# Kernel tuning notes

Hardware: AMD Instinct MI355X
Metric: run time of the kernel (lower is better)

## Reference

```python
import jax, jax.numpy as jnp
import numpy as np

HEAD_DIM = 128
ROPE_THETA = 10000.0


def _rope_cos_sin(positions, head_dim, theta):
    # positions: [T] int -> cos/sin [T, head_dim] (LLaMA half-split convention)
    inv_freq = 1.0 / (theta ** (jnp.arange(0, head_dim, 2, dtype=jnp.float32) / head_dim))
    ang = positions.astype(jnp.float32)[:, None] * inv_freq  # [T, D/2]
    cos = jnp.concatenate([jnp.cos(ang), jnp.cos(ang)], axis=-1)
    sin = jnp.concatenate([jnp.sin(ang), jnp.sin(ang)], axis=-1)
    return cos, sin


def _apply_rope(x, cos, sin):
    # x: [T, H, D]; rotate_half: (-x2, x1)
    half = x.shape[-1] // 2
    rot = jnp.concatenate([-x[..., half:], x[..., :half]], axis=-1)
    return x * cos[:, None, :] + rot * sin[:, None, :]


def setup_inputs() -> dict:
    key = jax.random.key(0)
    ks = jax.random.split(key, 5)
    T, hid = 4096, 4096
    S = 1024  # equal-length sequences -> B = T // S = 4
    Hq, Hk, D = 32, 8, HEAD_DIM
    hidden = jax.random.normal(ks[0], (T, hid), dtype=jnp.float32)
    positions = (jnp.arange(T, dtype=jnp.int32) % S)
    q_w = jax.random.normal(ks[1], (Hq * D, hid), dtype=jnp.float32) * 0.02
    k_w = jax.random.normal(ks[2], (Hk * D, hid), dtype=jnp.float32) * 0.02
    v_w = jax.random.normal(ks[3], (Hk * D, hid), dtype=jnp.float32) * 0.02
    o_w = jax.random.normal(ks[4], (hid, Hq * D), dtype=jnp.float32) * 0.02
    return {"hidden": hidden, "positions": positions, "q_w": q_w, "k_w": k_w,
            "v_w": v_w, "o_w": o_w, "seq_len": S}


def reference(hidden, positions, q_w, k_w, v_w, o_w, seq_len):
    T, hid = hidden.shape
    D = HEAD_DIM
    Hq = q_w.shape[0] // D
    Hk = k_w.shape[0] // D
    G = Hq // Hk  # num_kv_groups
    S = int(seq_len)
    B = T // S
    # QKV projections (ColumnParallel, tp=1): y = x @ W^T
    q = (hidden @ q_w.T).reshape(T, Hq, D)
    k = (hidden @ k_w.T).reshape(T, Hk, D)
    v = (hidden @ v_w.T).reshape(T, Hk, D)
    # fused RoPE on q and k
    cos, sin = _rope_cos_sin(positions, D, ROPE_THETA)
    q = _apply_rope(q, cos, sin)
    k = _apply_rope(k, cos, sin)
    # varlen (equal-length) causal GQA attention
    q = q.reshape(B, S, Hk, G, D)
    k = k.reshape(B, S, Hk, D)
    v = v.reshape(B, S, Hk, D)
    scale = 1.0 / np.sqrt(D).astype(np.float32)
    scores = jnp.einsum('bqhgd,bkhd->bhgqk', q, k) * scale  # [B,Hk,G,S,S]
    causal = jnp.tril(jnp.ones((S, S), dtype=bool))
    scores = jnp.where(causal, scores, jnp.asarray(-1e30, scores.dtype))
    attn = jax.nn.softmax(scores, axis=-1)
    out = jnp.einsum('bhgqk,bkhd->bqhgd', attn, v).reshape(T, Hq * D)
    # output projection (RowParallel, tp=1)
    return out @ o_w.T
```

## Files before the change

### kernel.cpp

```cpp
#include <hip/hip_runtime.h>
#include <hip/hip_bf16.h>

typedef __attribute__((ext_vector_type(8))) short bf16x8;
typedef __attribute__((ext_vector_type(4))) float f32x4;
typedef __attribute__((ext_vector_type(8))) unsigned short u16x8;

__device__ inline unsigned short f2bf(float f) {
  unsigned u = __builtin_bit_cast(unsigned, f);
  u += 0x7FFFu + ((u >> 16) & 1u);
  return (unsigned short)(u >> 16);
}
__device__ inline float b2f(unsigned short h) {
  unsigned u = ((unsigned)h) << 16;
  return __builtin_bit_cast(float, u);
}

typedef const __attribute__((address_space(1))) void* gas_ptr;
typedef __attribute__((address_space(3))) void* las_ptr;
__device__ inline void load_lds16(const void* g, void* l) {
  __builtin_amdgcn_global_load_lds((gas_ptr)g, (las_ptr)l, 16, 0, 0);
}

#define PHB() do { asm volatile("" ::: "memory"); __builtin_amdgcn_s_barrier(); \
                   __builtin_amdgcn_sched_barrier(0); } while (0)
#define PHB_MID() do { asm volatile("" ::: "memory"); __builtin_amdgcn_s_barrier(); } while (0)

__global__ __launch_bounds__(256) void cvt_f32_bf16(const float* __restrict__ src,
                                                    unsigned short* __restrict__ dst,
                                                    int n4) {
  int i = blockIdx.x * 256 + threadIdx.x;
  if (i >= n4) return;
  float4 v = ((const float4*)src)[i];
  ushort4 o;
  o.x = f2bf(v.x); o.y = f2bf(v.y); o.z = f2bf(v.z); o.w = f2bf(v.w);
  ((ushort4*)dst)[i] = o;
}

template <int NLOADS>
__device__ inline void stage_tile(const unsigned short* __restrict__ g, int ld,
                                  size_t grow0, int kcol0, char* ldsdst, int tid) {
#pragma unroll
  for (int i = 0; i < NLOADS; ++i) {
    int c = tid + i * 512;
    int r = c >> 3;
    int k = (c & 7) ^ (r & 7);
    load_lds16(g + (grow0 + r) * ld + kcol0 + k * 8, ldsdst + c * 16);
  }
}

template <int Kc, int Nc>
__global__ __launch_bounds__(512, 1) void gemmQ(const unsigned short* __restrict__ A,
                                                const unsigned short* __restrict__ B,
                                                unsigned short* __restrict__ C) {
  __shared__ __attribute__((aligned(16))) char lds[98304];
  const int tid = threadIdx.x;
  const int wave = tid >> 6, lane = tid & 63;
  const int l15 = lane & 15, l4 = lane >> 4;
  const int wr = wave >> 2, wc = wave & 3;
  const int nTN = Nc >> 8;
  const int cpx = gridDim.x >> 3;
  const int orig = blockIdx.x;
  const int wg = (orig & 7) * cpx + (orig >> 3);
  const int bm = wg / nTN, bn = wg % nTN;
  const size_t rowA0 = (size_t)bm << 7, rowB0 = (size_t)bn << 8;
  const int nt = Kc >> 6;

  stage_tile<2>(A, Kc, rowA0, 0,  lds + 0,     tid);
  stage_tile<4>(B, Kc, rowB0, 0,  lds + 16384, tid);
  stage_tile<2>(A, Kc, rowA0, 64, lds + 49152, tid);
  stage_tile<4>(B, Kc, rowB0, 64, lds + 65536, tid);
  asm volatile("s_waitcnt vmcnt(6)" ::: "memory");
  __builtin_amdgcn_s_barrier();
  __builtin_amdgcn_sched_barrier(0);

  f32x4 acc[4][4] = {};

#pragma unroll 2
  for (int t = 0; t < nt; ++t) {
    char* cbuf = lds + (t & 1) * 49152;
    const char* bufA = cbuf;
    const char* bufB = cbuf + 16384;
    const int kc2 = (t + 2) << 6;

    bf16x8 af[4][2], bf[4][2];

#pragma unroll
    for (int m = 0; m < 2; ++m) {
      int row = wr * 64 + m * 16 + l15;
#pragma unroll
      for (int kk = 0; kk < 2; ++kk)
        af[m][kk] = *(const bf16x8*)(bufA + (row << 7) + (((kk * 4 + l4) ^ (row & 7)) << 4));
    }
#pragma unroll
    for (int n = 0; n < 2; ++n) {
      int row = wc * 64 + n * 16 + l15;
#pragma unroll
      for (int kk = 0; kk < 2; ++kk)
        bf[n][kk] = *(const bf16x8*)(bufB + (row << 7) + (((kk * 4 + l4) ^ (row & 7)) << 4));
    }
    PHB_MID();
    __builtin_amdgcn_s_setprio(1);
#pragma unroll
    for (int m = 0; m < 2; ++m)
#pragma unroll
      for (int n = 0; n < 2; ++n)
#pragma unroll
        for (int kk = 0; kk < 2; ++kk)
          acc[m][n] = __builtin_amdgcn_mfma_f32_16x16x32_bf16(af[m][kk], bf[n][kk], acc[m][n], 0, 0, 0);
    __builtin_amdgcn_s_setprio(0);
    PHB();

#pragma unroll
    for (int n = 2; n < 4; ++n) {
      int row = wc * 64 + n * 16 + l15;
#pragma unroll
      for (int kk = 0; kk < 2; ++kk)
        bf[n][kk] = *(const bf16x8*)(bufB + (row << 7) + (((kk * 4 + l4) ^ (row & 7)) << 4));
    }
    PHB_MID();
    __builtin_amdgcn_s_setprio(1);
#pragma unroll
    for (int m = 0; m < 2; ++m)
#pragma unroll
      for (int n = 2; n < 4; ++n)
#pragma unroll
        for (int kk = 0; kk < 2; ++kk)
          acc[m][n] = __builtin_amdgcn_mfma_f32_16x16x32_bf16(af[m][kk], bf[n][kk], acc[m][n], 0, 0, 0);
    __builtin_amdgcn_s_setprio(0);
    PHB();

#pragma unroll
    for (int m = 2; m < 4; ++m) {
      int row = wr * 64 + m * 16 + l15;
#pragma unroll
      for (int kk = 0; kk < 2; ++kk)
        af[m][kk] = *(const bf16x8*)(bufA + (row << 7) + (((kk * 4 + l4) ^ (row & 7)) << 4));
    }
    if (t < nt - 2) stage_tile<4>(B, Kc, rowB0, kc2, cbuf + 16384, tid);
    PHB_MID();
    __builtin_amdgcn_s_setprio(1);
#pragma unroll
    for (int m = 2; m < 4; ++m)
#pragma unroll
      for (int n = 0; n < 2; ++n)
#pragma unroll
        for (int kk = 0; kk < 2; ++kk)
          acc[m][n] = __builtin_amdgcn_mfma_f32_16x16x32_bf16(af[m][kk], bf[n][kk], acc[m][n], 0, 0, 0);
    __builtin_amdgcn_s_setprio(0);
    PHB();

    if (t < nt - 2) stage_tile<2>(A, Kc, rowA0, kc2, cbuf, tid);
    if (t <= nt - 3) { asm volatile("s_waitcnt vmcnt(6)" ::: "memory"); }
    else             { asm volatile("s_waitcnt vmcnt(0)" ::: "memory"); }
    PHB_MID();
    __builtin_amdgcn_s_setprio(1);
#pragma unroll
    for (int m = 2; m < 4; ++m)
#pragma unroll
      for (int n = 2; n < 4; ++n)
#pragma unroll
        for (int kk = 0; kk < 2; ++kk)
          acc[m][n] = __builtin_amdgcn_mfma_f32_16x16x32_bf16(af[m][kk], bf[n][kk], acc[m][n], 0, 0, 0);
    __builtin_amdgcn_s_setprio(0);
    PHB();
  }

#pragma unroll
  for (int m = 0; m < 4; ++m)
#pragma unroll
    for (int n = 0; n < 4; ++n)
#pragma unroll
      for (int r = 0; r < 4; ++r) {
        size_t row = rowA0 + wr * 64 + m * 16 + l4 * 4 + r;
        size_t col = rowB0 + wc * 64 + n * 16 + l15;
        C[row * Nc + col] = f2bf(acc[m][n][r]);
      }
}

__device__ inline void stage_half(const unsigned short* __restrict__ g, int ld,
                                  size_t grow0, int kcol0, char* ldsdst, int tid) {
#pragma unroll
  for (int i = 0; i < 2; ++i) {
    int c = tid + i * 512;
    int r = c >> 3;
    int k = (c & 7) ^ (r & 7);
    load_lds16(g + (grow0 + r) * ld + kcol0 + k * 8, ldsdst + c * 16);
  }
}

template <int Kc, int Nc, bool OUT_F32>
__global__ __launch_bounds__(512, 2) void gemm8(const unsigned short* __restrict__ A,
                                                const unsigned short* __restrict__ B,
                                                void* __restrict__ Cv) {
  __shared__ __attribute__((aligned(16))) char lds[131072];
  const int tid = threadIdx.x;
  const int wave = tid >> 6, lane = tid & 63;
  const int l15 = lane & 15, l4 = lane >> 4, swz = l15 & 7;
  const int wr = wave >> 2, wc = wave & 3;
  const int nTN = Nc >> 8;
  const int cpx = gridDim.x >> 3;
  const int orig = blockIdx.x;
  const int wg = (orig & 7) * cpx + (orig >> 3);
  const int bm = wg / nTN, bn = wg % nTN;
  const size_t rowA0 = (size_t)bm << 8, rowB0 = (size_t)bn << 8;
  const int nt = Kc >> 6;
  const int brow = (wc & 1) * 64;

  stage_half(A, Kc, rowA0,       0,  lds + 0,             tid);
  stage_half(A, Kc, rowA0 + 128, 0,  lds + 16384,         tid);
  stage_half(B, Kc, rowB0,       0,  lds + 32768,         tid);
  stage_half(B, Kc, rowB0 + 128, 0,  lds + 49152,         tid);
  stage_half(B, Kc, rowB0,       64, lds + 65536 + 32768, tid);
  stage_half(A, Kc, rowA0,       64, lds + 65536,         tid);
  stage_half(A, Kc, rowA0 + 128, 64, lds + 65536 + 16384, tid);
  asm volatile("s_waitcnt vmcnt(6)" ::: "memory");
  __builtin_amdgcn_s_barrier();
  __builtin_amdgcn_sched_barrier(0);

  f32x4 acc[8][4] = {};
  bf16x8 bf01[2][2];
  {
    const char* bufB0 = lds + 32768 + (wc >> 1) * 16384;
#pragma unroll
    for (int n = 0; n < 2; ++n)
#pragma unroll
      for (int kk = 0; kk < 2; ++kk)
        bf01[n][kk] = *(const bf16x8*)(bufB0 + ((brow + n * 16 + l15) << 7) + (((kk * 4 + l4) ^ swz) << 4));
  }

#pragma unroll 2
  for (int t = 0; t < nt; ++t) {
    char* cbuf = lds + (t & 1) * 65536;
    char* obuf = lds + ((t + 1) & 1) * 65536;
    const char* bufA = cbuf + wr * 16384;
    const char* bufB = cbuf + 32768 + (wc >> 1) * 16384;
    const int kc1 = (t + 1) << 6, kc2 = (t + 2) << 6;

    bf16x8 af[8][2], bf23[2][2];

#pragma unroll
    for (int m = 0; m < 4; ++m)
#pragma unroll
      for (int kk = 0; kk < 2; ++kk)
        af[m][kk] = *(const bf16x8*)(bufA + ((m * 16 + l15) << 7) + (((kk * 4 + l4) ^ swz) << 4));
    if (t < nt - 1) stage_half(B, Kc, rowB0 + 128, kc1, obuf + 49152, tid);
    PHB_MID();
    __builtin_amdgcn_s_setprio(1);
#pragma unroll
    for (int m = 0; m < 4; ++m)
#pragma unroll
      for (int n = 0; n < 2; ++n)
#pragma unroll
        for (int kk = 0; kk < 2; ++kk)
          acc[m][n] = __builtin_amdgcn_mfma_f32_16x16x32_bf16(af[m][kk], bf01[n][kk], acc[m][n], 0, 0, 0);
    __builtin_amdgcn_s_setprio(0);
    PHB();

#pragma unroll
    for (int n = 0; n < 2; ++n)
#pragma unroll
      for (int kk = 0; kk < 2; ++kk)
        bf23[n][kk] = *(const bf16x8*)(bufB + ((brow + (n + 2) * 16 + l15) << 7) + (((kk * 4 + l4) ^ swz) << 4));
    PHB_MID();
    __builtin_amdgcn_s_setprio(1);
#pragma unroll
    for (int m = 0; m < 4; ++m)
#pragma unroll
      for (int n = 0; n < 2; ++n)
#pragma unroll
        for (int kk = 0; kk < 2; ++kk)
          acc[m][n + 2] = __builtin_amdgcn_mfma_f32_16x16x32_bf16(af[m][kk], bf23[n][kk], acc[m][n + 2], 0, 0, 0);
    __builtin_amdgcn_s_setprio(0);
    PHB();

#pragma unroll
    for (int m = 4; m < 8; ++m)
#pragma unroll
      for (int kk = 0; kk < 2; ++kk)
        af[m][kk] = *(const bf16x8*)(bufA + ((m * 16 + l15) << 7) + (((kk * 4 + l4) ^ swz) << 4));
    if (t < nt - 2) stage_half(B, Kc, rowB0, kc2, cbuf + 32768, tid);
    PHB_MID();
    __builtin_amdgcn_s_setprio(1);
#pragma unroll
    for (int m = 4; m < 8; ++m)
#pragma unroll
      for (int n = 0; n < 2; ++n)
#pragma unroll
        for (int kk = 0; kk < 2; ++kk)
          acc[m][n] = __builtin_amdgcn_mfma_f32_16x16x32_bf16(af[m][kk], bf01[n][kk], acc[m][n], 0, 0, 0);
    __builtin_amdgcn_s_setprio(0);
    PHB();

    if (t < nt - 2) {
      stage_half(A, Kc, rowA0,       kc2, cbuf,         tid);
      stage_half(A, Kc, rowA0 + 128, kc2, cbuf + 16384, tid);
    }
    if (t <= nt - 3) { asm volatile("s_waitcnt vmcnt(8)" ::: "memory"); }
    else             { asm volatile("s_waitcnt vmcnt(0)" ::: "memory"); }
    PHB_MID();
    if (t < nt - 1) {
      const char* bufB1 = obuf + 32768 + (wc >> 1) * 16384;
#pragma unroll
      for (int n = 0; n < 2; ++n)
#pragma unroll
        for (int kk = 0; kk < 2; ++kk)
          bf01[n][kk] = *(const bf16x8*)(bufB1 + ((brow + n * 16 + l15) << 7) + (((kk * 4 + l4) ^ swz) << 4));
    }
    __builtin_amdgcn_s_setprio(1);
#pragma unroll
    for (int m = 4; m < 8; ++m)
#pragma unroll
      for (int n = 0; n < 2; ++n)
#pragma unroll
        for (int kk = 0; kk < 2; ++kk)
          acc[m][n + 2] = __builtin_amdgcn_mfma_f32_16x16x32_bf16(af[m][kk], bf23[n][kk], acc[m][n + 2], 0, 0, 0);
    __builtin_amdgcn_s_setprio(0);
    PHB();
  }

#pragma unroll
  for (int m = 0; m < 8; ++m)
#pragma unroll
    for (int n = 0; n < 4; ++n)
#pragma unroll
      for (int r = 0; r < 4; ++r) {
        size_t row = rowA0 + wr * 128 + m * 16 + l4 * 4 + r;
        size_t col = rowB0 + wc * 64 + n * 16 + l15;
        float v = acc[m][n][r];
        if (OUT_F32) ((float*)Cv)[row * Nc + col] = v;
        else         ((unsigned short*)Cv)[row * Nc + col] = f2bf(v);
      }
}

__global__ __launch_bounds__(256) void rope_kernel(unsigned short* __restrict__ qkv,
                                                   const int* __restrict__ positions) {
  int gw = (blockIdx.x * 256 + threadIdx.x) >> 6;
  int lane = threadIdx.x & 63;
  int t = gw / 40, h = gw % 40;
  size_t col0 = (h < 32) ? ((size_t)h << 7) : (4096 + ((size_t)(h - 32) << 7));
  unsigned short* p = qkv + (size_t)t * 6144 + col0;
  float pos = (float)positions[t];
  float inv = powf(10000.0f, -(float)lane * (1.0f / 64.0f));
  float ang = pos * inv;
  float s, c;
  sincosf(ang, &s, &c);
  float x1 = b2f(p[lane]);
  float x2 = b2f(p[lane + 64]);
  p[lane]      = f2bf(x1 * c - x2 * s);
  p[lane + 64] = f2bf(x2 * c + x1 * s);
}

__global__ __launch_bounds__(256, 4) void attn_kernel(const unsigned short* __restrict__ qkv,
                                                      unsigned short* __restrict__ ao) {
  int orig = blockIdx.x;
  int wgid = (orig & 7) * 128 + (orig >> 3);
  int pair = wgid & 7;
  int hq = (wgid >> 3) & 31;
  int b  = wgid >> 8;
  int hk = hq >> 2;
  int tid = threadIdx.x, wave = tid >> 6, lane = tid & 63;
  int l15 = lane & 15, l4 = lane >> 4;

  __shared__ __attribute__((aligned(16))) char ldsA[16384];
  __shared__ __attribute__((aligned(16))) unsigned short Vt[128][72];
  unsigned short (*Ks)[128]    = (unsigned short (*)[128])ldsA;
  unsigned short (*Ps)[16][72] = (unsigned short (*)[16][72])ldsA;

  const float scale = 0.08838834764831845f;

#pragma unroll 1
  for (int iq = 0; iq < 2; ++iq) {
    const int qa = iq ? (15 - pair) : pair;
    const size_t qrow0 = (size_t)(b * 1024 + qa * 64 + wave * 16);

    bf16x8 qf[4];
    {
      const unsigned short* qp = qkv + (qrow0 + l15) * 6144 + ((size_t)hq << 7) + l4 * 8;
#pragma unroll
      for (int kc = 0; kc < 4; ++kc) qf[kc] = *(const bf16x8*)(qp + kc * 32);
    }

    float m_i[4], l_i[4];
    f32x4 oacc[8];
#pragma unroll
    for (int r = 0; r < 4; ++r) { m_i[r] = -1e30f; l_i[r] = 0.0f; }
#pragma unroll
    for (int d = 0; d < 8; ++d) oacc[d] = f32x4{0.f, 0.f, 0.f, 0.f};

#pragma unroll 1
    for (int kt = 0; kt <= qa; ++kt) {
      __syncthreads();

      const unsigned short* kbase = qkv + (size_t)(b * 1024 + kt * 64) * 6144 + 4096 + ((size_t)hk << 7);
#pragma unroll
      for (int j = 0; j < 4; ++j) {
        int c = (j * 4 + wave) * 64 + lane;
        int r = c >> 4;
        int cc = (c & 15) ^ (r & 7);
        load_lds16(kbase + (size_t)r * 6144 + cc * 8, ldsA + c * 16);
      }
      {
        const unsigned short* vp = qkv + (size_t)(b * 1024 + kt * 64 + lane) * 6144 + 5120 + ((size_t)hk << 7) + wave * 32;
        u16x8 va0 = *(const u16x8*)(vp);
        u16x8 va1 = *(const u16x8*)(vp + 8);
        u16x8 va2 = *(const u16x8*)(vp + 16);
        u16x8 va3 = *(const u16x8*)(vp + 24);
        int d0 = wave * 32;
#pragma unroll
        for (int c = 0; c < 8; ++c) Vt[d0 + c][lane]      = va0[c];
#pragma unroll
        for (int c = 0; c < 8; ++c) Vt[d0 + 8 + c][lane]  = va1[c];
#pragma unroll
        for (int c = 0; c < 8; ++c) Vt[d0 + 16 + c][lane] = va2[c];
#pragma unroll
        for (int c = 0; c < 8; ++c) Vt[d0 + 24 + c][lane] = va3[c];
      }
      __syncthreads();

      float pbuf[4][4];
      float tmax[4] = {-1e30f, -1e30f, -1e30f, -1e30f};
#pragma unroll
      for (int nt = 0; nt < 4; ++nt) {
        f32x4 sacc = {0.f, 0.f, 0.f, 0.f};
        int row = nt * 16 + l15;
#pragma unroll
        for (int kc = 0; kc < 4; ++kc) {
          const unsigned short* kp = &Ks[0][0] + row * 128 + (((kc * 4 + l4) ^ (row & 7)) * 8);
          bf16x8 kf = *(const bf16x8*)kp;
          sacc = __builtin_amdgcn_mfma_f32_16x16x32_bf16(qf[kc], kf, sacc, 0, 0, 0);
        }
#pragma unroll
        for (int r = 0; r < 4; ++r) {
          float s = sacc[r] * scale;
          if (kt == qa) {
            int kcol = nt * 16 + l15;
            int qrow = wave * 16 + l4 * 4 + r;
            if (kcol > qrow) s = -1e30f;
          }
          pbuf[nt][r] = s;
          tmax[r] = fmaxf(tmax[r], s);
        }
      }
      __syncthreads();

#pragma unroll
      for (int r = 0; r < 4; ++r) {
        float v = tmax[r];
        v = fmaxf(v, __shfl_xor(v, 1));
        v = fmaxf(v, __shfl_xor(v, 2));
        v = fmaxf(v, __shfl_xor(v, 4));
        v = fmaxf(v, __shfl_xor(v, 8));
        tmax[r] = v;
      }
      float rescale[4];
#pragma unroll
      for (int r = 0; r < 4; ++r) {
        float mn = fmaxf(m_i[r], tmax[r]);
        rescale[r] = __expf(m_i[r] - mn);
        m_i[r] = mn;
      }
      float psum[4] = {0.f, 0.f, 0.f, 0.f};
#pragma unroll
      for (int nt = 0; nt < 4; ++nt)
#pragma unroll
        for (int r = 0; r < 4; ++r) {
          float p = __expf(pbuf[nt][r] - m_i[r]);
          pbuf[nt][r] = p;
          psum[r] += p;
        }
#pragma unroll
      for (int r = 0; r < 4; ++r) {
        float v = psum[r];
        v += __shfl_xor(v, 1);
        v += __shfl_xor(v, 2);
        v += __shfl_xor(v, 4);
        v += __shfl_xor(v, 8);
        l_i[r] = l_i[r] * rescale[r] + v;
      }
#pragma unroll
      for (int d = 0; d < 8; ++d)
#pragma unroll
        for (int r = 0; r < 4; ++r) oacc[d][r] *= rescale[r];

#pragma unroll
      for (int nt = 0; nt < 4; ++nt)
#pragma unroll
        for (int r = 0; r < 4; ++r)
          Ps[wave][l4 * 4 + r][nt * 16 + l15] = f2bf(pbuf[nt][r]);

#pragma unroll
      for (int h = 0; h < 2; ++h) {
        bf16x8 pa = *(const bf16x8*)&Ps[wave][l15][h * 32 + l4 * 8];
#pragma unroll
        for (int d = 0; d < 8; ++d) {
          bf16x8 vf = *(const bf16x8*)&Vt[d * 16 + l15][h * 32 + l4 * 8];
          oacc[d] = __builtin_amdgcn_mfma_f32_16x16x32_bf16(pa, vf, oacc[d], 0, 0, 0);
        }
      }
    }

#pragma unroll
    for (int d = 0; d < 8; ++d)
#pragma unroll
      for (int r = 0; r < 4; ++r) {
        size_t row = qrow0 + l4 * 4 + r;
        size_t col = ((size_t)hq << 7) + d * 16 + l15;
        ao[row * 4096 + col] = f2bf(oacc[d][r] / l_i[r]);
      }
  }
}

extern "C" void kernel_launch(void* const* d_in, const int* in_sizes, int n_in,
                              void* d_out, int out_size, void* d_ws, size_t ws_size,
                              hipStream_t stream) {
  const float* hidden    = (const float*)d_in[0];
  const int*   positions = (const int*)d_in[1];
  const float* q_w       = (const float*)d_in[2];
  const float* k_w       = (const float*)d_in[3];
  const float* v_w       = (const float*)d_in[4];
  const float* o_w       = (const float*)d_in[5];
  float* out = (float*)d_out;

  char* ws = (char*)d_ws;
  unsigned short* hidB  = (unsigned short*)(ws);
  unsigned short* wqkvB = (unsigned short*)(ws + 33554432);
  unsigned short* woB   = (unsigned short*)(ws + 83886080);
  unsigned short* qkvB  = (unsigned short*)(ws + 117440512);
  unsigned short* aoB   = (unsigned short*)(ws + 167772160);

  cvt_f32_bf16<<<16384, 256, 0, stream>>>(hidden, hidB, 4194304);
  cvt_f32_bf16<<<16384, 256, 0, stream>>>(q_w, wqkvB, 4194304);
  cvt_f32_bf16<<<4096, 256, 0, stream>>>(k_w, wqkvB + 16777216, 1048576);
  cvt_f32_bf16<<<4096, 256, 0, stream>>>(v_w, wqkvB + 20971520, 1048576);
  cvt_f32_bf16<<<16384, 256, 0, stream>>>(o_w, woB, 4194304);

  gemmQ<4096, 6144><<<768, 512, 0, stream>>>(hidB, wqkvB, qkvB);

  rope_kernel<<<40960, 256, 0, stream>>>(qkvB, positions);

  attn_kernel<<<1024, 256, 0, stream>>>(qkvB, aoB);

  gemm8<4096, 4096, true><<<256, 512, 0, stream>>>(aoB, woB, (void*)out);
}
```

Measured before the change: 546.1 us.

## Triple-buffer QKV GEMM pipeline and use 2D XCD-aware tile mapping

The QKV projection GEMM goes from a double-buffered LDS ring to a three-stage ring. Prefetches for step t+2 now go into a separate buffer, so each iteration needs two barrier phases instead of four, and all A fragments are loaded up front. A new xcd_decode maps block IDs so each XCD gets a contiguous 2D sub-grid of tiles, intended to improve L2 reuse, and the output GEMM uses the same mapping. This costs more LDS (144KB) and more live registers for fragments, and the new LDS waits and barriers may expose load latency differently.

```diff
diff --git a/kernel.cpp b/kernel.cpp
--- a/kernel.cpp
+++ b/kernel.cpp
@@ -48,36 +48,42 @@
   }
 }
 
-template <int Kc, int Nc>
-__global__ __launch_bounds__(512, 1) void gemmQ(const unsigned short* __restrict__ A,
+__device__ inline void xcd_decode(int orig, int nTM, int nTN, int& bm, int& bn) {
+  int x = orig & 7, i = orig >> 3;
+  int xr = x >> 1, xc = x & 1;
+  int bmch = nTM >> 2, bnch = nTN >> 1;
+  bm = xr * bmch + i / bnch;
+  bn = xc * bnch + i % bnch;
+}
+
+template <int Kc, int Nc, int Mc, bool OUT_F32>
+__global__ __launch_bounds__(512, 1) void gemmT(const unsigned short* __restrict__ A,
                                                 const unsigned short* __restrict__ B,
-                                                unsigned short* __restrict__ C) {
-  __shared__ __attribute__((aligned(16))) char lds[98304];
+                                                void* __restrict__ Cv) {
+  __shared__ __attribute__((aligned(16))) char lds[147456];
   const int tid = threadIdx.x;
   const int wave = tid >> 6, lane = tid & 63;
   const int l15 = lane & 15, l4 = lane >> 4;
   const int wr = wave >> 2, wc = wave & 3;
-  const int nTN = Nc >> 8;
-  const int cpx = gridDim.x >> 3;
-  const int orig = blockIdx.x;
-  const int wg = (orig & 7) * cpx + (orig >> 3);
-  const int bm = wg / nTN, bn = wg % nTN;
+  int bm, bn;
+  xcd_decode(blockIdx.x, Mc >> 7, Nc >> 8, bm, bn);
   const size_t rowA0 = (size_t)bm << 7, rowB0 = (size_t)bn << 8;
   const int nt = Kc >> 6;
 
-  stage_tile<2>(A, Kc, rowA0, 0,  lds + 0,     tid);
-  stage_tile<4>(B, Kc, rowB0, 0,  lds + 16384, tid);
-  stage_tile<2>(A, Kc, rowA0, 64, lds + 49152, tid);
-  stage_tile<4>(B, Kc, rowB0, 64, lds + 65536, tid);
+  stage_tile<2>(A, Kc, rowA0, 0,  lds + 0,             tid);
+  stage_tile<4>(B, Kc, rowB0, 0,  lds + 16384,         tid);
+  stage_tile<2>(A, Kc, rowA0, 64, lds + 49152,         tid);
+  stage_tile<4>(B, Kc, rowB0, 64, lds + 49152 + 16384, tid);
   asm volatile("s_waitcnt vmcnt(6)" ::: "memory");
   __builtin_amdgcn_s_barrier();
   __builtin_amdgcn_sched_barrier(0);
 
   f32x4 acc[4][4] = {};
 
-#pragma unroll 2
+#pragma unroll 3
   for (int t = 0; t < nt; ++t) {
-    char* cbuf = lds + (t & 1) * 49152;
+    char* cbuf = lds + (t % 3) * 49152;
+    char* sbuf = lds + ((t + 2) % 3) * 49152;
     const char* bufA = cbuf;
     const char* bufB = cbuf + 16384;
     const int kc2 = (t + 2) << 6;
@@ -85,7 +91,7 @@
     bf16x8 af[4][2], bf[4][2];
 
 #pragma unroll
-    for (int m = 0; m < 2; ++m) {
+    for (int m = 0; m < 4; ++m) {
       int row = wr * 64 + m * 16 + l15;
 #pragma unroll
       for (int kk = 0; kk < 2; ++kk)
@@ -98,10 +104,13 @@
       for (int kk = 0; kk < 2; ++kk)
         bf[n][kk] = *(const bf16x8*)(bufB + (row << 7) + (((kk * 4 + l4) ^ (row & 7)) << 4));
     }
-    PHB_MID();
+    if (t < nt - 2) stage_tile<4>(B, Kc, rowB0, kc2, sbuf + 16384, tid);
+    __builtin_amdgcn_s_barrier();
+    asm volatile("s_waitcnt lgkmcnt(0)" ::: "memory");
+    __builtin_amdgcn_sched_barrier(0);
     __builtin_amdgcn_s_setprio(1);
 #pragma unroll
-    for (int m = 0; m < 2; ++m)
+    for (int m = 0; m < 4; ++m)
 #pragma unroll
       for (int n = 0; n < 2; ++n)
 #pragma unroll
@@ -117,45 +126,15 @@
       for (int kk = 0; kk < 2; ++kk)
         bf[n][kk] = *(const bf16x8*)(bufB + (row << 7) + (((kk * 4 + l4) ^ (row & 7)) << 4));
     }
-    PHB_MID();
-    __builtin_amdgcn_s_setprio(1);
-#pragma unroll
-    for (int m = 0; m < 2; ++m)
-#pragma unroll
-      for (int n = 2; n < 4; ++n)
-#pragma unroll
-        for (int kk = 0; kk < 2; ++kk)
-          acc[m][n] = __builtin_amdgcn_mfma_f32_16x16x32_bf16(af[m][kk], bf[n][kk], acc[m][n], 0, 0, 0);
-    __builtin_amdgcn_s_setprio(0);
-    PHB();
-
-#pragma unroll
-    for (int m = 2; m < 4; ++m) {
-      int row = wr * 64 + m * 16 + l15;
-#pragma unroll
-      for (int kk = 0; kk < 2; ++kk)
-        af[m][kk] = *(const bf16x8*)(bufA + (row << 7) + (((kk * 4 + l4) ^ (row & 7)) << 4));
-    }
-    if (t < nt - 2) stage_tile<4>(B, Kc, rowB0, kc2, cbuf + 16384, tid);
-    PHB_MID();
-    __builtin_amdgcn_s_setprio(1);
-#pragma unroll
-    for (int m = 2; m < 4; ++m)
-#pragma unroll
-      for (int n = 0; n < 2; ++n)
-#pragma unroll
-        for (int kk = 0; kk < 2; ++kk)
-          acc[m][n] = __builtin_amdgcn_mfma_f32_16x16x32_bf16(af[m][kk], bf[n][kk], acc[m][n], 0, 0, 0);
-    __builtin_amdgcn_s_setprio(0);
-    PHB();
-
-    if (t < nt - 2) stage_tile<2>(A, Kc, rowA0, kc2, cbuf, tid);
+    if (t < nt - 2) stage_tile<2>(A, Kc, rowA0, kc2, sbuf, tid);
     if (t <= nt - 3) { asm volatile("s_waitcnt vmcnt(6)" ::: "memory"); }
     else             { asm volatile("s_waitcnt vmcnt(0)" ::: "memory"); }
-    PHB_MID();
+    __builtin_amdgcn_s_barrier();
+    asm volatile("s_waitcnt lgkmcnt(0)" ::: "memory");
+    __builtin_amdgcn_sched_barrier(0);
     __builtin_amdgcn_s_setprio(1);
 #pragma unroll
-    for (int m = 2; m < 4; ++m)
+    for (int m = 0; m < 4; ++m)
 #pragma unroll
       for (int n = 2; n < 4; ++n)
 #pragma unroll
@@ -173,7 +152,9 @@
       for (int r = 0; r < 4; ++r) {
         size_t row = rowA0 + wr * 64 + m * 16 + l4 * 4 + r;
         size_t col = rowB0 + wc * 64 + n * 16 + l15;
-        C[row * Nc + col] = f2bf(acc[m][n][r]);
+        float v = acc[m][n][r];
+        if (OUT_F32) ((float*)Cv)[row * Nc + col] = v;
+        else         ((unsigned short*)Cv)[row * Nc + col] = f2bf(v);
       }
 }
 
@@ -188,7 +169,7 @@
   }
 }
 
-template <int Kc, int Nc, bool OUT_F32>
+template <int Kc, int Nc, int Mc, bool OUT_F32>
 __global__ __launch_bounds__(512, 2) void gemm8(const unsigned short* __restrict__ A,
                                                 const unsigned short* __restrict__ B,
                                                 void* __restrict__ Cv) {
@@ -197,11 +178,8 @@
   const int wave = tid >> 6, lane = tid & 63;
   const int l15 = lane & 15, l4 = lane >> 4, swz = l15 & 7;
   const int wr = wave >> 2, wc = wave & 3;
-  const int nTN = Nc >> 8;
-  const int cpx = gridDim.x >> 3;
-  const int orig = blockIdx.x;
-  const int wg = (orig & 7) * cpx + (orig >> 3);
-  const int bm = wg / nTN, bn = wg % nTN;
+  int bm, bn;
+  xcd_decode(blockIdx.x, Mc >> 8, Nc >> 8, bm, bn);
   const size_t rowA0 = (size_t)bm << 8, rowB0 = (size_t)bn << 8;
   const int nt = Kc >> 6;
   const int brow = (wc & 1) * 64;
@@ -534,11 +512,11 @@
   cvt_f32_bf16<<<4096, 256, 0, stream>>>(v_w, wqkvB + 20971520, 1048576);
   cvt_f32_bf16<<<16384, 256, 0, stream>>>(o_w, woB, 4194304);
 
-  gemmQ<4096, 6144><<<768, 512, 0, stream>>>(hidB, wqkvB, qkvB);
+  gemmT<4096, 6144, 4096, false><<<768, 512, 0, stream>>>(hidB, wqkvB, (void*)qkvB);
 
   rope_kernel<<<40960, 256, 0, stream>>>(qkvB, positions);
 
   attn_kernel<<<1024, 256, 0, stream>>>(qkvB, aoB);
 
-  gemm8<4096, 4096, true><<<256, 512, 0, stream>>>(aoB, woB, (void*)out);
-}
+  gemm8<4096, 4096, 4096, true><<<256, 512, 0, stream>>>(aoB, woB, (void*)out);
+}
```

New measurement: 521.8 us. -4.5%, faster.
